# Optimization experiments

Measured on AMD Instinct MI355X. Metric: run time of the kernel, lower is better.

## Reference

```python
import jax, jax.numpy as jnp
import numpy as np

N, C = 262144, 128
BN_EPS = 1e-5


def setup_inputs() -> dict:
    key = jax.random.key(0)
    ks = jax.random.split(key, 9)
    s = 1.0 / np.sqrt(C)  # torch Linear default init scale
    return {
        "x": jax.random.normal(ks[0], (N, C), dtype=jnp.float32),
        "W1": jax.random.uniform(ks[1], (C, C), jnp.float32, -s, s),
        "b1": jax.random.uniform(ks[2], (C,), jnp.float32, -s, s),
        "gamma1": jnp.ones((C,), jnp.float32),
        "beta1": jnp.zeros((C,), jnp.float32),
        "W2": jax.random.uniform(ks[3], (C, C), jnp.float32, -s, s),
        "b2": jax.random.uniform(ks[4], (C,), jnp.float32, -s, s),
        "gamma2": jnp.ones((C,), jnp.float32),
        "beta2": jnp.zeros((C,), jnp.float32),
    }


def _batchnorm(h, gamma, beta):
    # training-mode BatchNorm1d: batch mean, biased variance, eps=1e-5
    m = jnp.mean(h, axis=0)
    v = jnp.var(h, axis=0)
    return (h - m) * jax.lax.rsqrt(v + BN_EPS) * gamma + beta


def reference(x, W1, b1, gamma1, beta1, W2, b2, gamma2, beta2):
    res = x
    out = x @ W1.T + b1
    # contextNormalization: only the in-place `d -= mean` loop has effect
    # (return value is discarded in the original), i.e. mean-center over batch
    out = out - jnp.mean(out, axis=0)
    out = jax.nn.relu(_batchnorm(out, gamma1, beta1))
    out = out @ W2.T + b2
    out = out - jnp.mean(out, axis=0)
    out = jax.nn.relu(_batchnorm(out, gamma2, beta2))
    return out + res
```

## Files before the change

kernel.cpp:

```cpp
#include <hip/hip_runtime.h>
#include <hip/hip_bf16.h>

#define NROWS 262144
#define CDIM  128
#define BN_EPS 1e-5f
#define GGRID 1024
#define SROWS 32
#define SPB   (NROWS / SROWS / GGRID)

typedef __attribute__((ext_vector_type(8))) short bf16x8;
typedef __attribute__((ext_vector_type(4))) float f32x4;
#define LROW 136

static __device__ __forceinline__ unsigned int f2bf_rtn(float f) {
  unsigned int u = __float_as_uint(f);
  return (u + 0x7fffu + ((u >> 16) & 1u)) >> 16;
}
static __device__ __forceinline__ float bf2f(unsigned int b) {
  return __uint_as_float(b << 16);
}

template <bool NORM>
__global__ void __launch_bounds__(256, 4)
gemm_bn(const float* __restrict__ in, const float* __restrict__ W,
        const float* __restrict__ bias,
        const float* __restrict__ scsh_in,
        float* __restrict__ hout, float* __restrict__ part)
{
  __shared__ __align__(16) short lds[2][2][SROWS][LROW];

  const int tid  = threadIdx.x;
  const int lane = tid & 63;
  const int wave = tid >> 6;
  const int l15  = lane & 15;
  const int lq   = lane >> 4;
  const int wcol = wave * 32;
  const int srow = tid >> 4;
  const int sk0  = (tid & 15) * 8;

  bf16x8 bh[2][4], bl[2][4];
#pragma unroll
  for (int jt = 0; jt < 2; ++jt) {
    const float* wrow = W + (wcol + jt * 16 + l15) * CDIM;
#pragma unroll
    for (int ks = 0; ks < 4; ++ks) {
      const int k0 = ks * 32 + lq * 8;
      f32x4 w0 = *(const f32x4*)(wrow + k0);
      f32x4 w1 = *(const f32x4*)(wrow + k0 + 4);
      float wv[8] = {w0.x,w0.y,w0.z,w0.w,w1.x,w1.y,w1.z,w1.w};
#pragma unroll
      for (int e = 0; e < 8; ++e) {
        unsigned int h = f2bf_rtn(wv[e]);
        bh[jt][ks][e] = (short)h;
        bl[jt][ks][e] = (short)f2bf_rtn(wv[e] - bf2f(h));
      }
    }
  }

  float scv[8], shv[8];
  if constexpr (NORM) {
#pragma unroll
    for (int e = 0; e < 8; ++e) {
      scv[e] = scsh_in[sk0 + e];
      shv[e] = scsh_in[CDIM + sk0 + e];
    }
  }

  const float bias0 = bias[wcol + l15];
  const float bias1 = bias[wcol + 16 + l15];
  float s0 = 0.f, s1 = 0.f, q0 = 0.f, q1 = 0.f;

  const int row0 = blockIdx.x * (SPB * SROWS);

  auto cvt_write = [&](int buf, int lrow, f32x4 g0, f32x4 g1) {
    float av[8] = {g0.x,g0.y,g0.z,g0.w,g1.x,g1.y,g1.z,g1.w};
    if constexpr (NORM) {
#pragma unroll
      for (int e = 0; e < 8; ++e)
        av[e] = fmaxf(av[e] * scv[e] + shv[e], 0.f);
    }
    bf16x8 hi, lo;
#pragma unroll
    for (int e = 0; e < 8; ++e) {
      unsigned int h = f2bf_rtn(av[e]);
      hi[e] = (short)h;
      lo[e] = (short)f2bf_rtn(av[e] - bf2f(h));
    }
    *(bf16x8*)&lds[buf][0][lrow][sk0] = hi;
    *(bf16x8*)&lds[buf][1][lrow][sk0] = lo;
  };

  {
    const float* a0 = in + (size_t)(row0 + srow) * CDIM + sk0;
    const float* a1 = in + (size_t)(row0 + 16 + srow) * CDIM + sk0;
    f32x4 g0 = *(const f32x4*)a0, g1 = *(const f32x4*)(a0 + 4);
    f32x4 g2 = *(const f32x4*)a1, g3 = *(const f32x4*)(a1 + 4);
    cvt_write(0, srow, g0, g1);
    cvt_write(0, srow + 16, g2, g3);
  }
  __syncthreads();

  for (int s = 0; s < SPB; ++s) {
    const int cur = s & 1;
    const int r0 = row0 + s * SROWS;

    f32x4 g0 = {0,0,0,0}, g1 = {0,0,0,0}, g2 = {0,0,0,0}, g3 = {0,0,0,0};
    const bool more = (s + 1 < SPB);
    if (more) {
      const float* a0 = in + (size_t)(r0 + SROWS + srow) * CDIM + sk0;
      const float* a1 = in + (size_t)(r0 + SROWS + 16 + srow) * CDIM + sk0;
      g0 = *(const f32x4*)a0; g1 = *(const f32x4*)(a0 + 4);
      g2 = *(const f32x4*)a1; g3 = *(const f32x4*)(a1 + 4);
    }

    f32x4 acc[2][2];
#pragma unroll
    for (int st = 0; st < 2; ++st)
#pragma unroll
      for (int jt = 0; jt < 2; ++jt)
        acc[st][jt] = (f32x4){0.f,0.f,0.f,0.f};

#pragma unroll
    for (int st = 0; st < 2; ++st) {
#pragma unroll
      for (int ks = 0; ks < 4; ++ks) {
        const int kc = ks * 32 + lq * 8;
        bf16x8 ah = *(const bf16x8*)&lds[cur][0][st * 16 + l15][kc];
        bf16x8 al = *(const bf16x8*)&lds[cur][1][st * 16 + l15][kc];
        acc[st][0] = __builtin_amdgcn_mfma_f32_16x16x32_bf16(al, bh[0][ks], acc[st][0], 0, 0, 0);
        acc[st][0] = __builtin_amdgcn_mfma_f32_16x16x32_bf16(ah, bl[0][ks], acc[st][0], 0, 0, 0);
        acc[st][0] = __builtin_amdgcn_mfma_f32_16x16x32_bf16(ah, bh[0][ks], acc[st][0], 0, 0, 0);
        acc[st][1] = __builtin_amdgcn_mfma_f32_16x16x32_bf16(al, bh[1][ks], acc[st][1], 0, 0, 0);
        acc[st][1] = __builtin_amdgcn_mfma_f32_16x16x32_bf16(ah, bl[1][ks], acc[st][1], 0, 0, 0);
        acc[st][1] = __builtin_amdgcn_mfma_f32_16x16x32_bf16(ah, bh[1][ks], acc[st][1], 0, 0, 0);
      }
    }

    if (more) {
      cvt_write(cur ^ 1, srow, g0, g1);
      cvt_write(cur ^ 1, srow + 16, g2, g3);
    }
    __syncthreads();

#pragma unroll
    for (int st = 0; st < 2; ++st) {
      float* op = hout + (size_t)(r0 + st * 16 + lq * 4) * CDIM + wcol + l15;
#pragma unroll
      for (int r = 0; r < 4; ++r) {
        float h0 = acc[st][0][r] + bias0;
        float h1 = acc[st][1][r] + bias1;
        s0 += h0; q0 += h0 * h0;
        s1 += h1; q1 += h1 * h1;
        op[r * CDIM] = h0;
        op[r * CDIM + 16] = h1;
      }
    }
  }

  s0 += __shfl_xor(s0, 16); s0 += __shfl_xor(s0, 32);
  s1 += __shfl_xor(s1, 16); s1 += __shfl_xor(s1, 32);
  q0 += __shfl_xor(q0, 16); q0 += __shfl_xor(q0, 32);
  q1 += __shfl_xor(q1, 16); q1 += __shfl_xor(q1, 32);
  float* pb = part + (size_t)blockIdx.x * 256;
  if (lane < 16) {
    pb[wcol + lane]              = s0;
    pb[wcol + 16 + lane]         = s1;
    pb[CDIM + wcol + lane]       = q0;
    pb[CDIM + wcol + 16 + lane]  = q1;
  }
}

__global__ void __launch_bounds__(256)
bn_stats(const float* __restrict__ part, const float* __restrict__ gamma,
         const float* __restrict__ beta, float* __restrict__ scsh)
{
  const int c = blockIdx.x;
  const int t = threadIdx.x;
  float s = 0.f, q = 0.f;
  for (int b = t; b < GGRID; b += 256) {
    s += part[(size_t)b * 256 + c];
    q += part[(size_t)b * 256 + CDIM + c];
  }
  __shared__ float rs[256], rq[256];
  rs[t] = s; rq[t] = q;
  __syncthreads();
#pragma unroll
  for (int off = 128; off >= 1; off >>= 1) {
    if (t < off) { rs[t] += rs[t + off]; rq[t] += rq[t + off]; }
    __syncthreads();
  }
  if (t == 0) {
    const float inv_n = 1.0f / (float)NROWS;
    float m  = rs[0] * inv_n;
    float v  = rq[0] * inv_n - m * m;
    float sc = gamma[c] * rsqrtf(v + BN_EPS);
    scsh[c]        = sc;
    scsh[CDIM + c] = beta[c] - m * sc;
  }
}

__global__ void __launch_bounds__(256)
finalize(const f32x4* __restrict__ h2, const f32x4* __restrict__ xin,
         const float* __restrict__ scsh, f32x4* __restrict__ outp)
{
  const int tid0 = blockIdx.x * blockDim.x + threadIdx.x;
  const int c0 = (tid0 * 4) & (CDIM - 1);

  float sc[4], sh[4];
#pragma unroll
  for (int e = 0; e < 4; ++e) {
    sc[e] = scsh[c0 + e];
    sh[e] = scsh[CDIM + c0 + e];
  }

  const int n4 = NROWS * CDIM / 4;
  const int GR = gridDim.x * blockDim.x;
  for (int base = tid0; base < n4; base += GR * 4) {
    f32x4 h[4], xv[4], o[4];
#pragma unroll
    for (int u = 0; u < 4; ++u) {
      h[u]  = h2[base + u * GR];
      xv[u] = __builtin_nontemporal_load(&xin[base + u * GR]);
    }
#pragma unroll
    for (int u = 0; u < 4; ++u) {
      o[u].x = fmaxf(h[u].x * sc[0] + sh[0], 0.f) + xv[u].x;
      o[u].y = fmaxf(h[u].y * sc[1] + sh[1], 0.f) + xv[u].y;
      o[u].z = fmaxf(h[u].z * sc[2] + sh[2], 0.f) + xv[u].z;
      o[u].w = fmaxf(h[u].w * sc[3] + sh[3], 0.f) + xv[u].w;
    }
#pragma unroll
    for (int u = 0; u < 4; ++u)
      __builtin_nontemporal_store(o[u], &outp[base + u * GR]);
  }
}

extern "C" void kernel_launch(void* const* d_in, const int* in_sizes, int n_in,
                              void* d_out, int out_size, void* d_ws, size_t ws_size,
                              hipStream_t stream) {
  (void)in_sizes; (void)n_in; (void)out_size; (void)ws_size;
  const float* x   = (const float*)d_in[0];
  const float* W1  = (const float*)d_in[1];
  const float* b1  = (const float*)d_in[2];
  const float* g1  = (const float*)d_in[3];
  const float* be1 = (const float*)d_in[4];
  const float* W2  = (const float*)d_in[5];
  const float* b2  = (const float*)d_in[6];
  const float* g2  = (const float*)d_in[7];
  const float* be2 = (const float*)d_in[8];

  float* hbuf  = (float*)d_out;
  float* part1 = (float*)d_ws;
  float* part2 = part1 + (size_t)GGRID * 256;
  float* scsh1 = part2 + (size_t)GGRID * 256;
  float* scsh2 = scsh1 + 256;

  gemm_bn<false><<<GGRID, 256, 0, stream>>>(x, W1, b1, nullptr, hbuf, part1);
  bn_stats<<<CDIM, 256, 0, stream>>>(part1, g1, be1, scsh1);
  gemm_bn<true><<<GGRID, 256, 0, stream>>>(hbuf, W2, b2, scsh1, hbuf, part2);
  bn_stats<<<CDIM, 256, 0, stream>>>(part2, g2, be2, scsh2);
  finalize<<<4096, 256, 0, stream>>>((const f32x4*)hbuf, (const f32x4*)x,
                                     scsh2, (f32x4*)d_out);
}
```

Measured before the change: 456.7 us.

## Stage GEMM output through LDS and prefetch input two steps ahead

The GEMM+BN kernel now processes 16-row steps instead of 32 and prefetches global input two steps ahead using rotating register sets. Output tiles are staged in an LDS buffer so each row is written with coalesced, nontemporal 16-byte stores instead of scattered 4-byte stores. The finalize kernel also reads h2 with nontemporal loads. In exchange there is an extra barrier per step, more LDS use, and half the MFMA work per barrier.

After: 477.8 us. 4.6% more time.

```diff
diff --git a/kernel.cpp b/kernel.cpp
--- a/kernel.cpp
+++ b/kernel.cpp
@@ -5,8 +5,7 @@
 #define CDIM  128
 #define BN_EPS 1e-5f
 #define GGRID 1024
-#define SROWS 32
-#define SPB   (NROWS / SROWS / GGRID)
+#define SPB   (NROWS / 16 / GGRID)
 
 typedef __attribute__((ext_vector_type(8))) short bf16x8;
 typedef __attribute__((ext_vector_type(4))) float f32x4;
@@ -27,7 +26,8 @@
         const float* __restrict__ scsh_in,
         float* __restrict__ hout, float* __restrict__ part)
 {
-  __shared__ __align__(16) short lds[2][2][SROWS][LROW];
+  __shared__ __align__(16) short lds[2][2][16][LROW];
+  __shared__ __align__(16) float cstg[16][CDIM];
 
   const int tid  = threadIdx.x;
   const int lane = tid & 63;
@@ -70,9 +70,15 @@
   const float bias1 = bias[wcol + 16 + l15];
   float s0 = 0.f, s1 = 0.f, q0 = 0.f, q1 = 0.f;
 
-  const int row0 = blockIdx.x * (SPB * SROWS);
-
-  auto cvt_write = [&](int buf, int lrow, f32x4 g0, f32x4 g1) {
+  const int row0 = blockIdx.x * (SPB * 16);
+
+  auto loadS = [&](int s, f32x4& g0, f32x4& g1) {
+    const float* ap = in + (size_t)(row0 + s * 16 + srow) * CDIM + sk0;
+    g0 = *(const f32x4*)ap;
+    g1 = *(const f32x4*)(ap + 4);
+  };
+
+  auto cvt_write = [&](int buf, f32x4 g0, f32x4 g1) {
     float av[8] = {g0.x,g0.y,g0.z,g0.w,g1.x,g1.y,g1.z,g1.w};
     if constexpr (NORM) {
 #pragma unroll
@@ -86,75 +92,63 @@
       hi[e] = (short)h;
       lo[e] = (short)f2bf_rtn(av[e] - bf2f(h));
     }
-    *(bf16x8*)&lds[buf][0][lrow][sk0] = hi;
-    *(bf16x8*)&lds[buf][1][lrow][sk0] = lo;
+    *(bf16x8*)&lds[buf][0][srow][sk0] = hi;
+    *(bf16x8*)&lds[buf][1][srow][sk0] = lo;
   };
 
-  {
-    const float* a0 = in + (size_t)(row0 + srow) * CDIM + sk0;
-    const float* a1 = in + (size_t)(row0 + 16 + srow) * CDIM + sk0;
-    f32x4 g0 = *(const f32x4*)a0, g1 = *(const f32x4*)(a0 + 4);
-    f32x4 g2 = *(const f32x4*)a1, g3 = *(const f32x4*)(a1 + 4);
-    cvt_write(0, srow, g0, g1);
-    cvt_write(0, srow + 16, g2, g3);
-  }
+  auto body = [&](int s, f32x4& gA0, f32x4& gA1, f32x4& gB0, f32x4& gB1) {
+    const int cur = s & 1;
+    const int r0 = row0 + s * 16;
+
+    if (s + 2 < SPB) loadS(s + 2, gA0, gA1);
+
+    f32x4 acc0 = {0.f,0.f,0.f,0.f};
+    f32x4 acc1 = {0.f,0.f,0.f,0.f};
+#pragma unroll
+    for (int ks = 0; ks < 4; ++ks) {
+      const int kc = ks * 32 + lq * 8;
+      bf16x8 ah = *(const bf16x8*)&lds[cur][0][l15][kc];
+      bf16x8 al = *(const bf16x8*)&lds[cur][1][l15][kc];
+      acc0 = __builtin_amdgcn_mfma_f32_16x16x32_bf16(al, bh[0][ks], acc0, 0, 0, 0);
+      acc0 = __builtin_amdgcn_mfma_f32_16x16x32_bf16(ah, bl[0][ks], acc0, 0, 0, 0);
+      acc0 = __builtin_amdgcn_mfma_f32_16x16x32_bf16(ah, bh[0][ks], acc0, 0, 0, 0);
+      acc1 = __builtin_amdgcn_mfma_f32_16x16x32_bf16(al, bh[1][ks], acc1, 0, 0, 0);
+      acc1 = __builtin_amdgcn_mfma_f32_16x16x32_bf16(ah, bl[1][ks], acc1, 0, 0, 0);
+      acc1 = __builtin_amdgcn_mfma_f32_16x16x32_bf16(ah, bh[1][ks], acc1, 0, 0, 0);
+    }
+
+    if (s + 1 < SPB) cvt_write(cur ^ 1, gB0, gB1);
+    __syncthreads();
+
+#pragma unroll
+    for (int r = 0; r < 4; ++r) {
+      float h0 = acc0[r] + bias0;
+      float h1 = acc1[r] + bias1;
+      s0 += h0; q0 += h0 * h0;
+      s1 += h1; q1 += h1 * h1;
+      cstg[lq * 4 + r][wcol + l15]      = h0;
+      cstg[lq * 4 + r][wcol + 16 + l15] = h1;
+    }
+    __syncthreads();
+    const int srow2 = tid >> 5;
+    const int schk  = tid & 31;
+#pragma unroll
+    for (int p = 0; p < 2; ++p) {
+      f32x4 v = *(const f32x4*)&cstg[p * 8 + srow2][schk * 4];
+      __builtin_nontemporal_store(
+          v, (f32x4*)(hout + (size_t)(r0 + p * 8 + srow2) * CDIM + schk * 4));
+    }
+  };
+
+  f32x4 pA0, pA1, pB0, pB1;
+  loadS(0, pA0, pA1);
+  cvt_write(0, pA0, pA1);
+  loadS(1, pB0, pB1);
   __syncthreads();
 
-  for (int s = 0; s < SPB; ++s) {
-    const int cur = s & 1;
-    const int r0 = row0 + s * SROWS;
-
-    f32x4 g0 = {0,0,0,0}, g1 = {0,0,0,0}, g2 = {0,0,0,0}, g3 = {0,0,0,0};
-    const bool more = (s + 1 < SPB);
-    if (more) {
-      const float* a0 = in + (size_t)(r0 + SROWS + srow) * CDIM + sk0;
-      const float* a1 = in + (size_t)(r0 + SROWS + 16 + srow) * CDIM + sk0;
-      g0 = *(const f32x4*)a0; g1 = *(const f32x4*)(a0 + 4);
-      g2 = *(const f32x4*)a1; g3 = *(const f32x4*)(a1 + 4);
-    }
-
-    f32x4 acc[2][2];
-#pragma unroll
-    for (int st = 0; st < 2; ++st)
-#pragma unroll
-      for (int jt = 0; jt < 2; ++jt)
-        acc[st][jt] = (f32x4){0.f,0.f,0.f,0.f};
-
-#pragma unroll
-    for (int st = 0; st < 2; ++st) {
-#pragma unroll
-      for (int ks = 0; ks < 4; ++ks) {
-        const int kc = ks * 32 + lq * 8;
-        bf16x8 ah = *(const bf16x8*)&lds[cur][0][st * 16 + l15][kc];
-        bf16x8 al = *(const bf16x8*)&lds[cur][1][st * 16 + l15][kc];
-        acc[st][0] = __builtin_amdgcn_mfma_f32_16x16x32_bf16(al, bh[0][ks], acc[st][0], 0, 0, 0);
-        acc[st][0] = __builtin_amdgcn_mfma_f32_16x16x32_bf16(ah, bl[0][ks], acc[st][0], 0, 0, 0);
-        acc[st][0] = __builtin_amdgcn_mfma_f32_16x16x32_bf16(ah, bh[0][ks], acc[st][0], 0, 0, 0);
-        acc[st][1] = __builtin_amdgcn_mfma_f32_16x16x32_bf16(al, bh[1][ks], acc[st][1], 0, 0, 0);
-        acc[st][1] = __builtin_amdgcn_mfma_f32_16x16x32_bf16(ah, bl[1][ks], acc[st][1], 0, 0, 0);
-        acc[st][1] = __builtin_amdgcn_mfma_f32_16x16x32_bf16(ah, bh[1][ks], acc[st][1], 0, 0, 0);
-      }
-    }
-
-    if (more) {
-      cvt_write(cur ^ 1, srow, g0, g1);
-      cvt_write(cur ^ 1, srow + 16, g2, g3);
-    }
-    __syncthreads();
-
-#pragma unroll
-    for (int st = 0; st < 2; ++st) {
-      float* op = hout + (size_t)(r0 + st * 16 + lq * 4) * CDIM + wcol + l15;
-#pragma unroll
-      for (int r = 0; r < 4; ++r) {
-        float h0 = acc[st][0][r] + bias0;
-        float h1 = acc[st][1][r] + bias1;
-        s0 += h0; q0 += h0 * h0;
-        s1 += h1; q1 += h1 * h1;
-        op[r * CDIM] = h0;
-        op[r * CDIM + 16] = h1;
-      }
-    }
+  for (int s = 0; s < SPB; s += 2) {
+    body(s,     pA0, pA1, pB0, pB1);
+    body(s + 1, pB0, pB1, pA0, pA1);
   }
 
   s0 += __shfl_xor(s0, 16); s0 += __shfl_xor(s0, 32);
@@ -219,7 +213,7 @@
     f32x4 h[4], xv[4], o[4];
 #pragma unroll
     for (int u = 0; u < 4; ++u) {
-      h[u]  = h2[base + u * GR];
+      h[u]  = __builtin_nontemporal_load(&h2[base + u * GR]);
       xv[u] = __builtin_nontemporal_load(&xin[base + u * GR]);
     }
 #pragma unroll
```
